# Performance work log

Hardware: AMD Instinct MI355X
Metric: run time of the kernel (lower is better)

## Reference

```python
import jax, jax.numpy as jnp
import numpy as np

P = 3   # patch_size
D = 7   # displacement window side (odd)
K = 4   # top-k
C = 32  # n_feat
B, H, W = 2, 64, 64
EPS = 1e-12  # F.normalize default eps


def _unfold(x, p):
    """torch F.unfold(x, p, padding=p//2) -> [b, c, p*p, h, w] (row-major patch offsets)."""
    b, c, h, w = x.shape
    pad = p // 2
    xp = jnp.pad(x, ((0, 0), (0, 0), (pad, pad), (pad, pad)))
    return jnp.stack([xp[:, :, i:i + h, j:j + w] for i in range(p) for j in range(p)], axis=2)


def setup_inputs() -> dict:
    key = jax.random.key(0)
    ks = jax.random.split(key, 6)
    feat_t = jax.random.normal(ks[0], (B, C, H, W), jnp.float32)
    feat_tm1 = jax.random.normal(ks[1], (B, C, H, W), jnp.float32)
    # aggregator: Conv2d(k, 1, 1) == weighted sum over k + bias
    agg_w = jax.random.normal(ks[2], (K,), jnp.float32) / K
    agg_b = jax.random.normal(ks[3], (), jnp.float32) * 0.01
    # w_proj: Conv2d(2c, c*p^2, 1) == pointwise linear
    wproj_w = jax.random.normal(ks[4], (C * P * P, 2 * C), jnp.float32) / np.sqrt(2 * C)
    wproj_b = jax.random.normal(ks[5], (C * P * P,), jnp.float32) * 0.01
    return dict(feat_t=feat_t, feat_tm1=feat_tm1, agg_w=agg_w, agg_b=agg_b,
                wproj_w=wproj_w, wproj_b=wproj_b)


def reference(feat_t, feat_tm1, agg_w, agg_b, wproj_w, wproj_b):
    b, c, h, w = feat_t.shape
    p2, d2 = P * P, D * D
    # 3x3 patch unfold of both frames -> [b, c*9, h, w]
    ft_u = _unfold(feat_t, P).reshape(b, c * p2, h, w)
    ftm1_u = _unfold(feat_tm1, P).reshape(b, c * p2, h, w)
    # displacement window over previous-frame patches -> [b, c*9, h, w, d^2]
    disp = jnp.moveaxis(_unfold(ftm1_u, D), 2, -1)
    # cosine similarity along the (c*9) descriptor axis
    ft_n = ft_u / jnp.maximum(jnp.linalg.norm(ft_u, axis=1, keepdims=True), EPS)
    dot = jnp.einsum('bchw,bchwd->bhwd', ft_n, disp)          # [b,h,w,d2]
    dnorm = jnp.maximum(jnp.linalg.norm(disp, axis=1), EPS)    # [b,h,w,d2]
    sim = dot / dnorm
    # top-k displacements per pixel, gather their patch descriptors
    _, idx = jax.lax.top_k(sim, K)                             # [b,h,w,K]
    idx_b = jnp.broadcast_to(idx[:, None], (b, c * p2, h, w, K))
    rel = jnp.take_along_axis(disp, idx_b, axis=-1)            # [b, c*9, h, w, K]
    rel = rel.reshape(b, c, p2, h, w, K)
    # aggregator 1x1 conv over k -> [b, c, h, w, p2]
    agg = jnp.einsum('bcphwk,k->bchwp', rel, agg_w) + agg_b
    # per-pixel patch weights from concatenated features
    cat = jnp.concatenate([feat_t, feat_tm1], axis=1)          # [b, 2c, h, w]
    wgt = jnp.einsum('bihw,oi->bohw', cat, wproj_w) + wproj_b[None, :, None, None]
    wgt = jnp.moveaxis(wgt.reshape(b, c, p2, h, w), 2, -1)     # [b, c, h, w, p2]
    return jnp.sum(agg * wgt, axis=-1)                         # [b, c, h, w]
```

## Files before the change

### kernel.cpp

```cpp
#include <hip/hip_runtime.h>

constexpr float EPSF = 1e-12f;

using short8 = __attribute__((ext_vector_type(8))) short;
using f32x4  = __attribute__((ext_vector_type(4))) float;

__device__ __forceinline__ unsigned short f2bf(float f) {
    unsigned int u = __float_as_uint(f);
    u += 0x7fffu + ((u >> 16) & 1u);
    return (unsigned short)(u >> 16);
}

__global__ __launch_bounds__(512, 4) void agg_mono(
    const float* __restrict__ ft, const float* __restrict__ f1,
    const float* __restrict__ agg_w, const float* __restrict__ agg_bp,
    const float* __restrict__ wproj_w, const float* __restrict__ wproj_b,
    float* __restrict__ out)
{
    __shared__ __align__(16) float pool[16254];
    __shared__ int chosb[16][4];

    float* qw   = pool;
    float* kw   = pool + 1944;
    float* wgtl = pool + 9720;
    float* Tb   = pool + 14904;
    float* Nb   = pool + 15884;
    float* rbnb = pool + 16100;
    unsigned short* Wb = reinterpret_cast<unsigned short*>(pool);
    unsigned short* Bb = reinterpret_cast<unsigned short*>(pool + 14392);

    const int t = threadIdx.x;
    const int pix0 = blockIdx.x << 4;
    const int b  = pix0 >> 12;
    const int y  = (pix0 >> 6) & 63;
    const int x0 = pix0 & 63;

    const float* ftb = ft + ((size_t)b << 17);
    const float* f1b = f1 + ((size_t)b << 17);

    float4 stgK4[4];
    #pragma unroll
    for (int s = 0; s < 4; ++s) {
        int slot = (s << 9) + t;
        if (slot < 1728) {
            int c4 = slot / 216, pos = slot - c4 * 216;
            int kr = pos / 24, kc = pos - kr * 24;
            int gy = y - 4 + kr, gx = x0 - 4 + kc;
            float4 v = {0.f, 0.f, 0.f, 0.f};
            if ((unsigned)gy < 64u && (unsigned)gx < 64u) {
                const float* p = f1b + ((size_t)(c4 << 2) << 12) + (gy << 6) + gx;
                v.x = p[0]; v.y = p[1 << 12]; v.z = p[2 << 12]; v.w = p[3 << 12];
            }
            stgK4[s] = v;
        }
    }
    float4 stgQ4 = {0.f, 0.f, 0.f, 0.f};
    if (t < 432) {
        int c4 = t / 54, pos = t - c4 * 54;
        int qr = pos / 18, qc = pos - qr * 18;
        int gy = y - 1 + qr, gx = x0 - 1 + qc;
        if ((unsigned)gy < 64u && (unsigned)gx < 64u) {
            const float* p = ftb + ((size_t)(c4 << 2) << 12) + (gy << 6) + gx;
            stgQ4.x = p[0]; stgQ4.y = p[1 << 12];
            stgQ4.z = p[2 << 12]; stgQ4.w = p[3 << 12];
        }
    }

    #pragma unroll
    for (int s = 0; s < 2; ++s) {
        int idx = (s << 9) + t;
        int i = idx >> 4, ppx = idx & 15;
        const float* src = (i < 32) ? ftb : f1b;
        float v = src[((size_t)(i & 31) << 12) + (y << 6) + x0 + ppx];
        Bb[(((i >> 3) << 4) + ppx) * 8 + (i & 7)] = f2bf(v);
    }

    {
        const float4* w4g = reinterpret_cast<const float4*>(wproj_w);
        #pragma unroll
        for (int s = 0; s < 9; ++s) {
            int f4 = (s << 9) + t;
            float4 wv = w4g[f4];
            int o = f4 >> 4, k4 = f4 & 15;
            int off = ((((o >> 4) << 3) + (k4 >> 1)) * 16 + (o & 15)) * 8
                    + ((k4 & 1) << 2);
            ushort4 bv;
            bv.x = f2bf(wv.x); bv.y = f2bf(wv.y);
            bv.z = f2bf(wv.z); bv.w = f2bf(wv.w);
            *reinterpret_cast<ushort4*>(&Wb[off]) = bv;
        }
    }
    __syncthreads();

    {
        const int lane = t & 63;
        const int wv8 = t >> 6;
        const int lr = lane & 15;
        const int lg = lane >> 4;
        short8 bf0 = *reinterpret_cast<const short8*>(&Bb[(lg * 16 + lr) * 8]);
        short8 bf1 = *reinterpret_cast<const short8*>(&Bb[((4 + lg) * 16 + lr) * 8]);
        #pragma unroll
        for (int ti = 0; ti < 3; ++ti) {
            if (ti == 2 && wv8 >= 2) break;
            const int tt = (ti == 0) ? wv8 : (ti == 1 ? wv8 + 8 : wv8 + 16);
            const float4 bias = *reinterpret_cast<const float4*>(
                wproj_b + tt * 16 + lg * 4);
            f32x4 acc;
            acc[0] = bias.x; acc[1] = bias.y; acc[2] = bias.z; acc[3] = bias.w;
            short8 a0 = *reinterpret_cast<const short8*>(
                &Wb[((tt * 8 + lg) * 16 + lr) * 8]);
            short8 a1 = *reinterpret_cast<const short8*>(
                &Wb[((tt * 8 + 4 + lg) * 16 + lr) * 8]);
            acc = __builtin_amdgcn_mfma_f32_16x16x32_bf16(a0, bf0, acc, 0, 0, 0);
            acc = __builtin_amdgcn_mfma_f32_16x16x32_bf16(a1, bf1, acc, 0, 0, 0);
            #pragma unroll
            for (int qi = 0; qi < 4; ++qi) {
                int o = tt * 16 + lg * 4 + qi;
                int cc = o / 9, jj = o - cc * 9;
                wgtl[lr * 292 + jj * 32 + cc] = acc[qi];
            }
        }
    }
    __syncthreads();

    #pragma unroll
    for (int s = 0; s < 4; ++s) {
        int slot = (s << 9) + t;
        if (slot < 1728) {
            int c4 = slot / 216, pos = slot - c4 * 216;
            *reinterpret_cast<float4*>(&kw[pos * 36 + (c4 << 2)]) = stgK4[s];
        }
    }
    if (t < 432) {
        int c4 = t / 54, pos = t - c4 * 54;
        *reinterpret_cast<float4*>(&qw[pos * 36 + (c4 << 2)]) = stgQ4;
    }
    __syncthreads();

    if (t < 216) {
        float s = 0.f;
        #pragma unroll
        for (int c4 = 0; c4 < 8; ++c4) {
            float4 v = *reinterpret_cast<const float4*>(&kw[t * 36 + (c4 << 2)]);
            s += v.x * v.x + v.y * v.y + v.z * v.z + v.w * v.w;
        }
        Nb[t] = s;
    }
    __syncthreads();
    if (t < 154) {
        int cyi = t / 22, cxi = t - cyi * 22;
        int kr = cyi + 1, kc = cxi + 1;
        float bn = 0.f;
        #pragma unroll
        for (int di = -1; di <= 1; ++di)
            #pragma unroll
            for (int dj = -1; dj <= 1; ++dj)
                bn += Nb[(kr + di) * 24 + kc + dj];
        rbnb[t] = 1.0f / fmaxf(sqrtf(bn), EPSF);
    }

    {
        const int g = t >> 3, c4 = t & 7;
        #pragma unroll
        for (int pr = 0; pr < 2; ++pr) {
            int p = (pr << 6) + g;
            if (p < 126) {
                int u = p / 18, xx = p - u * 18;
                float av[7] = {0.f, 0.f, 0.f, 0.f, 0.f, 0.f, 0.f};
                #pragma unroll
                for (int r = 0; r < 3; ++r) {
                    float4 qv = *reinterpret_cast<const float4*>(
                        &qw[(r * 18 + xx) * 36 + (c4 << 2)]);
                    #pragma unroll
                    for (int v = 0; v < 7; ++v) {
                        float4 kv = *reinterpret_cast<const float4*>(
                            &kw[((r + u) * 24 + xx + v) * 36 + (c4 << 2)]);
                        av[v] += qv.x * kv.x + qv.y * kv.y + qv.z * kv.z + qv.w * kv.w;
                    }
                }
                #pragma unroll
                for (int v = 0; v < 7; ++v) {
                    float s = av[v];
                    s += __shfl_xor(s, 1, 64);
                    s += __shfl_xor(s, 2, 64);
                    s += __shfl_xor(s, 4, 64);
                    if (c4 == 0) Tb[(u * 7 + v) * 20 + xx] = s;
                }
            }
        }
    }
    __syncthreads();

    {
        const int lane = t & 63;
        const int wvv = t >> 6;
        const int hf = lane >> 5;
        const int c = lane & 31;
        const int ppx = (wvv << 1) + hf;
        float s0 = 0.f, s1;
        {
            int u = c / 7, v = c - u * 7;
            int cy = y + u - 3, cx = x0 + ppx + v - 3;
            if ((unsigned)cy < 64u && (unsigned)cx < 64u) {
                float dot = Tb[c * 20 + ppx] + Tb[c * 20 + ppx + 1]
                          + Tb[c * 20 + ppx + 2];
                s0 = dot * rbnb[u * 22 + ppx + v];
            }
        }
        if (c < 17) {
            int d = c + 32;
            int u = d / 7, v = d - u * 7;
            int cy = y + u - 3, cx = x0 + ppx + v - 3;
            s1 = 0.f;
            if ((unsigned)cy < 64u && (unsigned)cx < 64u) {
                float dot = Tb[d * 20 + ppx] + Tb[d * 20 + ppx + 1]
                          + Tb[d * 20 + ppx + 2];
                s1 = dot * rbnb[u * 22 + ppx + v];
            }
        } else s1 = -3.0e38f;
        #pragma unroll
        for (int k = 0; k < 4; ++k) {
            float bs; int bi;
            if (s0 >= s1) { bs = s0; bi = c; }
            else          { bs = s1; bi = c + 32; }
            #pragma unroll
            for (int off = 16; off; off >>= 1) {
                float os = __shfl_xor(bs, off, 64);
                int   oi = __shfl_xor(bi, off, 64);
                if (os > bs || (os == bs && oi < bi)) { bs = os; bi = oi; }
            }
            if (c == 0) chosb[ppx][k] = bi;
            if (bi == c)           s0 = -3.0e38f;
            else if (bi == c + 32) s1 = -3.0e38f;
        }
    }
    __syncthreads();

    if (t < 128) {
        const int px = t & 15;
        const int c4 = t >> 4;
        const int co = c4 << 2;
        const float ab = agg_bp[0];
        float awv[4];
        #pragma unroll
        for (int k = 0; k < 4; ++k) awv[k] = agg_w[k];
        int uo[4], vo[4]; bool cval[4];
        #pragma unroll
        for (int k = 0; k < 4; ++k) {
            int d = chosb[px][k];
            int u = d / 7, v = d - u * 7;
            int cy = y + u - 3, cx = x0 + px + v - 3;
            cval[k] = ((unsigned)cy < 64u) && ((unsigned)cx < 64u);
            uo[k] = u; vo[k] = v;
        }
        float4 outv = {0.f, 0.f, 0.f, 0.f};
        #pragma unroll
        for (int j = 0; j < 9; ++j) {
            int pi = j / 3, pj = j - pi * 3;
            float4 g = {ab, ab, ab, ab};
            #pragma unroll
            for (int k = 0; k < 4; ++k) {
                if (cval[k]) {
                    float4 vv = *reinterpret_cast<const float4*>(
                        &kw[((uo[k] + pi) * 24 + px + vo[k] + pj) * 36 + co]);
                    g.x += awv[k] * vv.x; g.y += awv[k] * vv.y;
                    g.z += awv[k] * vv.z; g.w += awv[k] * vv.w;
                }
            }
            float4 wg = *reinterpret_cast<const float4*>(
                &wgtl[px * 292 + j * 32 + co]);
            outv.x += wg.x * g.x; outv.y += wg.y * g.y;
            outv.z += wg.z * g.z; outv.w += wg.w * g.w;
        }
        const size_t obase = ((size_t)((b << 5) + co) << 12) + (y << 6) + x0 + px;
        out[obase]              = outv.x;
        out[obase + (1u << 12)] = outv.y;
        out[obase + (2u << 12)] = outv.z;
        out[obase + (3u << 12)] = outv.w;
    }
}

extern "C" void kernel_launch(void* const* d_in, const int* in_sizes, int n_in,
                              void* d_out, int out_size, void* d_ws, size_t ws_size,
                              hipStream_t stream)
{
    const float* feat_t   = (const float*)d_in[0];
    const float* feat_tm1 = (const float*)d_in[1];
    const float* agg_w    = (const float*)d_in[2];
    const float* agg_b    = (const float*)d_in[3];
    const float* wproj_w  = (const float*)d_in[4];
    const float* wproj_b  = (const float*)d_in[5];
    float* outp = (float*)d_out;
    (void)d_ws; (void)ws_size;

    agg_mono<<<512, 512, 0, stream>>>(feat_t, feat_tm1, agg_w, agg_b,
                                      wproj_w, wproj_b, outp);
}
```

Before: 21.63 us.

## Warp-specialize block: 6 waves load K/Q windows while 2 waves compute projection

```diff
diff --git a/kernel.cpp b/kernel.cpp
--- a/kernel.cpp
+++ b/kernel.cpp
@@ -17,17 +17,15 @@
     const float* __restrict__ wproj_w, const float* __restrict__ wproj_b,
     float* __restrict__ out)
 {
-    __shared__ __align__(16) float pool[16254];
+    __shared__ __align__(16) float pool[15742];
     __shared__ int chosb[16][4];
 
     float* qw   = pool;
     float* kw   = pool + 1944;
     float* wgtl = pool + 9720;
-    float* Tb   = pool + 14904;
-    float* Nb   = pool + 15884;
-    float* rbnb = pool + 16100;
-    unsigned short* Wb = reinterpret_cast<unsigned short*>(pool);
-    unsigned short* Bb = reinterpret_cast<unsigned short*>(pool + 14392);
+    float* Tb   = pool + 14392;
+    float* Nb   = pool + 15372;
+    float* rbnb = pool + 15588;
 
     const int t = threadIdx.x;
     const int pix0 = blockIdx.x << 4;
@@ -38,79 +36,73 @@
     const float* ftb = ft + ((size_t)b << 17);
     const float* f1b = f1 + ((size_t)b << 17);
 
-    float4 stgK4[4];
-    #pragma unroll
-    for (int s = 0; s < 4; ++s) {
-        int slot = (s << 9) + t;
-        if (slot < 1728) {
-            int c4 = slot / 216, pos = slot - c4 * 216;
-            int kr = pos / 24, kc = pos - kr * 24;
-            int gy = y - 4 + kr, gx = x0 - 4 + kc;
-            float4 v = {0.f, 0.f, 0.f, 0.f};
-            if ((unsigned)gy < 64u && (unsigned)gx < 64u) {
-                const float* p = f1b + ((size_t)(c4 << 2) << 12) + (gy << 6) + gx;
-                v.x = p[0]; v.y = p[1 << 12]; v.z = p[2 << 12]; v.w = p[3 << 12];
-            }
-            stgK4[s] = v;
-        }
-    }
-    float4 stgQ4 = {0.f, 0.f, 0.f, 0.f};
-    if (t < 432) {
-        int c4 = t / 54, pos = t - c4 * 54;
-        int qr = pos / 18, qc = pos - qr * 18;
-        int gy = y - 1 + qr, gx = x0 - 1 + qc;
-        if ((unsigned)gy < 64u && (unsigned)gx < 64u) {
-            const float* p = ftb + ((size_t)(c4 << 2) << 12) + (gy << 6) + gx;
-            stgQ4.x = p[0]; stgQ4.y = p[1 << 12];
-            stgQ4.z = p[2 << 12]; stgQ4.w = p[3 << 12];
-        }
-    }
-
-    #pragma unroll
-    for (int s = 0; s < 2; ++s) {
-        int idx = (s << 9) + t;
-        int i = idx >> 4, ppx = idx & 15;
-        const float* src = (i < 32) ? ftb : f1b;
-        float v = src[((size_t)(i & 31) << 12) + (y << 6) + x0 + ppx];
-        Bb[(((i >> 3) << 4) + ppx) * 8 + (i & 7)] = f2bf(v);
-    }
-
-    {
-        const float4* w4g = reinterpret_cast<const float4*>(wproj_w);
-        #pragma unroll
-        for (int s = 0; s < 9; ++s) {
-            int f4 = (s << 9) + t;
-            float4 wv = w4g[f4];
-            int o = f4 >> 4, k4 = f4 & 15;
-            int off = ((((o >> 4) << 3) + (k4 >> 1)) * 16 + (o & 15)) * 8
-                    + ((k4 & 1) << 2);
-            ushort4 bv;
-            bv.x = f2bf(wv.x); bv.y = f2bf(wv.y);
-            bv.z = f2bf(wv.z); bv.w = f2bf(wv.w);
-            *reinterpret_cast<ushort4*>(&Wb[off]) = bv;
-        }
-    }
-    __syncthreads();
-
-    {
+    if (t < 384) {
+        #pragma unroll
+        for (int s = 0; s < 5; ++s) {
+            int slot = s * 384 + t;
+            if (slot < 1728) {
+                int c4 = slot / 216, pos = slot - c4 * 216;
+                int kr = pos / 24, kc = pos - kr * 24;
+                int gy = y - 4 + kr, gx = x0 - 4 + kc;
+                float4 v = {0.f, 0.f, 0.f, 0.f};
+                if ((unsigned)gy < 64u && (unsigned)gx < 64u) {
+                    const float* p = f1b + ((size_t)(c4 << 2) << 12) + (gy << 6) + gx;
+                    v.x = p[0]; v.y = p[1 << 12]; v.z = p[2 << 12]; v.w = p[3 << 12];
+                }
+                *reinterpret_cast<float4*>(&kw[pos * 36 + (c4 << 2)]) = v;
+            }
+        }
+        #pragma unroll
+        for (int s = 0; s < 2; ++s) {
+            int slot = s * 384 + t;
+            if (slot < 432) {
+                int c4 = slot / 54, pos = slot - c4 * 54;
+                int qr = pos / 18, qc = pos - qr * 18;
+                int gy = y - 1 + qr, gx = x0 - 1 + qc;
+                float4 v = {0.f, 0.f, 0.f, 0.f};
+                if ((unsigned)gy < 64u && (unsigned)gx < 64u) {
+                    const float* p = ftb + ((size_t)(c4 << 2) << 12) + (gy << 6) + gx;
+                    v.x = p[0]; v.y = p[1 << 12]; v.z = p[2 << 12]; v.w = p[3 << 12];
+                }
+                *reinterpret_cast<float4*>(&qw[pos * 36 + (c4 << 2)]) = v;
+            }
+        }
+    } else {
         const int lane = t & 63;
-        const int wv8 = t >> 6;
+        const int wv2 = (t >> 6) - 6;
         const int lr = lane & 15;
         const int lg = lane >> 4;
-        short8 bf0 = *reinterpret_cast<const short8*>(&Bb[(lg * 16 + lr) * 8]);
-        short8 bf1 = *reinterpret_cast<const short8*>(&Bb[((4 + lg) * 16 + lr) * 8]);
-        #pragma unroll
-        for (int ti = 0; ti < 3; ++ti) {
-            if (ti == 2 && wv8 >= 2) break;
-            const int tt = (ti == 0) ? wv8 : (ti == 1 ? wv8 + 8 : wv8 + 16);
+        short8 bf0, bf1;
+        {
+            const float* pft = ftb + (y << 6) + x0 + lr;
+            const float* pf1 = f1b + (y << 6) + x0 + lr;
+            #pragma unroll
+            for (int j = 0; j < 8; ++j) {
+                bf0[j] = (short)f2bf(pft[(size_t)(lg * 8 + j) << 12]);
+                bf1[j] = (short)f2bf(pf1[(size_t)(lg * 8 + j) << 12]);
+            }
+        }
+        #pragma unroll 3
+        for (int ti = 0; ti < 9; ++ti) {
+            const int tt = wv2 + 2 * ti;
+            const float* wrow = wproj_w + (size_t)(tt * 16 + lr) * 64 + lg * 8;
+            float4 wa = *reinterpret_cast<const float4*>(wrow);
+            float4 wb = *reinterpret_cast<const float4*>(wrow + 4);
+            float4 wc = *reinterpret_cast<const float4*>(wrow + 32);
+            float4 wd = *reinterpret_cast<const float4*>(wrow + 36);
+            short8 a0, a1;
+            a0[0] = (short)f2bf(wa.x); a0[1] = (short)f2bf(wa.y);
+            a0[2] = (short)f2bf(wa.z); a0[3] = (short)f2bf(wa.w);
+            a0[4] = (short)f2bf(wb.x); a0[5] = (short)f2bf(wb.y);
+            a0[6] = (short)f2bf(wb.z); a0[7] = (short)f2bf(wb.w);
+            a1[0] = (short)f2bf(wc.x); a1[1] = (short)f2bf(wc.y);
+            a1[2] = (short)f2bf(wc.z); a1[3] = (short)f2bf(wc.w);
+            a1[4] = (short)f2bf(wd.x); a1[5] = (short)f2bf(wd.y);
+            a1[6] = (short)f2bf(wd.z); a1[7] = (short)f2bf(wd.w);
             const float4 bias = *reinterpret_cast<const float4*>(
                 wproj_b + tt * 16 + lg * 4);
             f32x4 acc;
             acc[0] = bias.x; acc[1] = bias.y; acc[2] = bias.z; acc[3] = bias.w;
-            short8 a0 = *reinterpret_cast<const short8*>(
-                &Wb[((tt * 8 + lg) * 16 + lr) * 8]);
-            short8 a1 = *reinterpret_cast<const short8*>(
-                &Wb[((tt * 8 + 4 + lg) * 16 + lr) * 8]);
             acc = __builtin_amdgcn_mfma_f32_16x16x32_bf16(a0, bf0, acc, 0, 0, 0);
             acc = __builtin_amdgcn_mfma_f32_16x16x32_bf16(a1, bf1, acc, 0, 0, 0);
             #pragma unroll
@@ -123,20 +115,6 @@
     }
     __syncthreads();
 
-    #pragma unroll
-    for (int s = 0; s < 4; ++s) {
-        int slot = (s << 9) + t;
-        if (slot < 1728) {
-            int c4 = slot / 216, pos = slot - c4 * 216;
-            *reinterpret_cast<float4*>(&kw[pos * 36 + (c4 << 2)]) = stgK4[s];
-        }
-    }
-    if (t < 432) {
-        int c4 = t / 54, pos = t - c4 * 54;
-        *reinterpret_cast<float4*>(&qw[pos * 36 + (c4 << 2)]) = stgQ4;
-    }
-    __syncthreads();
-
     if (t < 216) {
         float s = 0.f;
         #pragma unroll
@@ -147,6 +125,7 @@
         Nb[t] = s;
     }
     __syncthreads();
+
     if (t < 154) {
         int cyi = t / 22, cxi = t - cyi * 22;
         int kr = cyi + 1, kc = cxi + 1;
@@ -158,7 +137,6 @@
                 bn += Nb[(kr + di) * 24 + kc + dj];
         rbnb[t] = 1.0f / fmaxf(sqrtf(bn), EPSF);
     }
-
     {
         const int g = t >> 3, c4 = t & 7;
         #pragma unroll
```

Result: slower. 22.28 us (+3.0%).
